# Kernel optimization log

Hardware: AMD Instinct MI355X
Metric: run time of the kernel (lower is better)

## Reference

```python
import jax, jax.numpy as jnp
import numpy as np

B, S, H, DH = 2, 2048, 16, 64
DIM = H * DH          # 1024
WIN = 512             # relpos_win_size
LN_EPS = 1e-5


def setup_inputs() -> dict:
    key = jax.random.key(0)
    ks = jax.random.split(key, 8)
    return {
        "q": jax.random.normal(ks[0], (B, S, H, DH), dtype=jnp.float32),
        "k": jax.random.normal(ks[1], (B, S, H, DH), dtype=jnp.float32),
        "relpos_emb": jax.random.normal(ks[2], (WIN, DIM), dtype=jnp.float32),
        "ln_scale": jnp.ones((DIM,), dtype=jnp.float32),
        "ln_bias": jnp.zeros((DIM,), dtype=jnp.float32),
        "Wq": jax.random.normal(ks[3], (DIM, DIM), dtype=jnp.float32),
        "bq": jnp.zeros((DIM,), dtype=jnp.float32),
        "Wk": jax.random.normal(ks[4], (DIM, DIM), dtype=jnp.float32),
        "bk": jnp.zeros((DIM,), dtype=jnp.float32),
    }


def reference(q, k, relpos_emb, ln_scale, ln_bias, Wq, bq, Wk, bk):
    b, nq, h, dh = q.shape
    nk = k.shape[1]
    win = relpos_emb.shape[0]

    # LayerNorm over the embedding dim (use_pos_layer_norm=True); dropout is identity (eval).
    mu = jnp.mean(relpos_emb, axis=-1, keepdims=True)
    var = jnp.mean(jnp.square(relpos_emb - mu), axis=-1, keepdims=True)
    pe = (relpos_emb - mu) * jax.lax.rsqrt(var + LN_EPS) * ln_scale + ln_bias

    qpos = jnp.arange(nq)
    kpos = jnp.arange(nk)
    rel = jnp.clip(kpos[None, :] - qpos[:, None], -(win - 1), 0) + (win - 1)
    idx = jnp.broadcast_to(rel[None, None, :, :], (b, h, nq, nk))

    # Linear projections of the (small) relpos table, split into heads.
    relpos_k = (pe @ Wk.T + bk).reshape(win, h, dh)  # relpos_k_proj
    relpos_q = (pe @ Wq.T + bq).reshape(win, h, dh)  # relpos_q_proj

    # query-to-position: scores over window then gather along window axis (dim 3).
    query_pos_scores = jnp.einsum('bnhx,khx->bhnk', q, relpos_k)
    logits_query_pos = jnp.take_along_axis(query_pos_scores, idx, axis=3)  # [b,h,nq,nk]

    key_pos_scores = jnp.einsum('bnhx,khx->bhkn', k, relpos_q)
    logits_pos_key = jnp.take_along_axis(key_pos_scores, idx, axis=2)      # [b,h,nq,nk]

    # scale_factor = 1 + True + True = 3 (static constant, omitted from array outputs)
    return logits_pos_key, logits_query_pos, relpos_q, relpos_k
```

## Files before the change

kernel.cpp:

```cpp
#include <hip/hip_runtime.h>

#define BB 2
#define S 2048
#define H 16
#define DH 64
#define DIM 1024
#define WIN 512

#define OUT_PK 0
#define OUT_QP 134217728
#define OUT_RQ 268435456
#define OUT_RK 268959744

#define WS_C0Q   1024
#define WS_C511Q (1024 + 65536)
#define WS_C0K   (1024 + 2*65536)
#define WS_C511K (1024 + 3*65536)
#define WS_BF_BASE 263168

typedef short bf16x8 __attribute__((ext_vector_type(8)));
typedef float f32x4 __attribute__((ext_vector_type(4)));

__device__ inline short f2bf(float f) {
    union { float f; unsigned int u; } cv; cv.f = f;
    unsigned int u = cv.u + 0x7FFFu + ((cv.u >> 16) & 1u);
    return (short)(u >> 16);
}

__device__ inline float bf2f(short s) {
    union { unsigned int u; float f; } cv;
    cv.u = ((unsigned int)(unsigned short)s) << 16;
    return cv.f;
}

__global__ __launch_bounds__(256) void prep1(const float* __restrict__ emb,
        const float* __restrict__ lnsc, const float* __restrict__ lnbi,
        const float* __restrict__ Wq, const float* __restrict__ bq,
        const float* __restrict__ Wk, const float* __restrict__ bk,
        const float* __restrict__ q, const float* __restrict__ k,
        float* __restrict__ out, short* __restrict__ rqbf, short* __restrict__ rkbf,
        short* __restrict__ qbf, short* __restrict__ kbf) {
    __shared__ short As[64 * 72];
    __shared__ short Bs[64 * 72];
    __shared__ float smu[64];
    __shared__ float srs[64];
    int bid = blockIdx.x;
    int t = threadIdx.x;

    if (bid >= 256) {
        int cb = bid - 256;
        int z = cb >> 10;
        int blk = cb & 1023;
        const float* src = z ? k : q;
        short* dst = z ? kbf : qbf;
        int e0 = (blk * 256 + t) * 16;
        int c = e0 & 63, hh = (e0 >> 6) & 15, n = (e0 >> 10) & 2047, b = e0 >> 21;
        short* dbase = dst + (((size_t)(b * 16 + hh) * 2048) + n) * 64 + c;
#pragma unroll
        for (int i = 0; i < 4; ++i) {
            float4 v = *reinterpret_cast<const float4*>(src + e0 + i * 4);
            short4 o = { f2bf(v.x), f2bf(v.y), f2bf(v.z), f2bf(v.w) };
            *reinterpret_cast<short4*>(dbase + i * 4) = o;
        }
        return;
    }

    int z = bid >> 7;
    int d0i = ((bid >> 6) & 1) * 8 + (bid & 7);
    int r0i = (bid >> 3) & 7;
    const float* W    = z ? Wk : Wq;
    const float* bias = z ? bk : bq;
    float* o = out + (z ? OUT_RK : OUT_RQ);
    short* bfo = z ? rkbf : rqbf;
    int r0 = r0i * 64;
    int d0 = d0i * 64;

    {
        int rr = t >> 2, p = t & 3;
        const float4* rp = reinterpret_cast<const float4*>(emb + (r0 + rr) * DIM + p * 256);
        float s = 0.f, sq = 0.f;
#pragma unroll
        for (int i = 0; i < 64; ++i) {
            float4 v = rp[i];
            s  += v.x + v.y + v.z + v.w;
            sq += v.x * v.x + v.y * v.y + v.z * v.z + v.w * v.w;
        }
        s += __shfl_xor(s, 1); sq += __shfl_xor(sq, 1);
        s += __shfl_xor(s, 2); sq += __shfl_xor(sq, 2);
        if (p == 0) {
            float mu = s / DIM;
            float var = sq / DIM - mu * mu;
            smu[rr] = mu;
            srs[rr] = rsqrtf(var + 1e-5f);
        }
    }
    __syncthreads();

    int lane = t & 63, w = t >> 6, lr = lane & 15, lg = lane >> 4;
    int srow = t >> 2, seg = (t & 3) * 16;
    float mu = smu[srow], rs = srs[srow];

    f32x4 acc[4] = {};
    for (int c0 = 0; c0 < DIM; c0 += 64) {
        const float4* ep = reinterpret_cast<const float4*>(emb + (size_t)(r0 + srow) * DIM + c0 + seg);
        const float4* wp = reinterpret_cast<const float4*>(W + (size_t)(d0 + srow) * DIM + c0 + seg);
        short4* ad = reinterpret_cast<short4*>(&As[srow * 72 + seg]);
        short4* wd = reinterpret_cast<short4*>(&Bs[srow * 72 + seg]);
#pragma unroll
        for (int i = 0; i < 4; ++i) {
            float4 v = ep[i], wv = wp[i];
            int cb2 = c0 + seg + i * 4;
            float4 sc = *reinterpret_cast<const float4*>(lnsc + cb2);
            float4 bi = *reinterpret_cast<const float4*>(lnbi + cb2);
            short4 a4 = { f2bf((v.x - mu) * rs * sc.x + bi.x),
                          f2bf((v.y - mu) * rs * sc.y + bi.y),
                          f2bf((v.z - mu) * rs * sc.z + bi.z),
                          f2bf((v.w - mu) * rs * sc.w + bi.w) };
            short4 w4 = { f2bf(wv.x), f2bf(wv.y), f2bf(wv.z), f2bf(wv.w) };
            ad[i] = a4;
            wd[i] = w4;
        }
        __syncthreads();
#pragma unroll
        for (int kk = 0; kk < 2; ++kk) {
            bf16x8 a = *reinterpret_cast<const bf16x8*>(&As[(w * 16 + lr) * 72 + kk * 32 + lg * 8]);
#pragma unroll
            for (int cg = 0; cg < 4; ++cg) {
                bf16x8 b = *reinterpret_cast<const bf16x8*>(&Bs[(cg * 16 + lr) * 72 + kk * 32 + lg * 8]);
                acc[cg] = __builtin_amdgcn_mfma_f32_16x16x32_bf16(a, b, acc[cg], 0, 0, 0);
            }
        }
        __syncthreads();
    }
#pragma unroll
    for (int cg = 0; cg < 4; ++cg) {
        int col = d0 + cg * 16 + lr;
        float bv = bias[col];
        int hh = col >> 6, cc = col & 63;
#pragma unroll
        for (int reg = 0; reg < 4; ++reg) {
            int rr = r0 + w * 16 + lg * 4 + reg;
            float val = acc[cg][reg] + bv;
            o[(size_t)rr * DIM + col] = val;
            bfo[((size_t)(hh * 512) + rr) * 64 + cc] = f2bf(val);
        }
    }
}

__global__ __launch_bounds__(256) void cvec(const short* __restrict__ qbf,
        const short* __restrict__ kbf, const short* __restrict__ rqbf,
        const short* __restrict__ rkbf, float* __restrict__ ws) {
    int cid = blockIdx.x;
    int z = cid >> 10;
    int rem = cid & 1023;
    int bh = rem >> 5, rb = rem & 31;
    int t = threadIdx.x;
    int rr = t >> 2, p = t & 3;
    int n = rb * 64 + rr;
    int h = bh & 15;
    const short* X = (z ? kbf : qbf) + ((size_t)bh * 2048 + n) * 64 + p * 16;
    const short* T = (z ? rqbf : rkbf) + (size_t)h * 512 * 64 + p * 16;
    bf16x8 x0 = *reinterpret_cast<const bf16x8*>(X);
    bf16x8 x1 = *reinterpret_cast<const bf16x8*>(X + 8);
    bf16x8 a0 = *reinterpret_cast<const bf16x8*>(T);
    bf16x8 a1 = *reinterpret_cast<const bf16x8*>(T + 8);
    bf16x8 c0 = *reinterpret_cast<const bf16x8*>(T + 511 * 64);
    bf16x8 c1 = *reinterpret_cast<const bf16x8*>(T + 511 * 64 + 8);
    float d0 = 0.f, d1 = 0.f;
#pragma unroll
    for (int e = 0; e < 8; ++e) {
        float xa = bf2f(x0[e]), xb = bf2f(x1[e]);
        d0 += xa * bf2f(a0[e]) + xb * bf2f(a1[e]);
        d1 += xa * bf2f(c0[e]) + xb * bf2f(c1[e]);
    }
    d0 += __shfl_xor(d0, 1); d0 += __shfl_xor(d0, 2);
    d1 += __shfl_xor(d1, 1); d1 += __shfl_xor(d1, 2);
    if (p == 0) {
        int o = bh * S + n;
        if (!z) { ws[WS_C0Q + o] = d0; ws[WS_C511Q + o] = d1; }
        else    { ws[WS_C0K + o] = d0; ws[WS_C511K + o] = d1; }
    }
}

__global__ __launch_bounds__(256) void outk(const short* __restrict__ qbf,
        const short* __restrict__ kbf, const short* __restrict__ rqbf,
        const short* __restrict__ rkbf, const float* __restrict__ ws,
        float* __restrict__ out) {
    __shared__ short Yt[128 * 68];

    int bid = blockIdx.x;
    int wid = (bid & 7) * 2984 + (bid >> 3);
    int panel = wid / 373, o = wid % 373;
    int PK = panel >> 5, bh = panel & 31, h = bh & 15;
    int t = threadIdx.x;
    float* obase = out + (PK ? OUT_PK : OUT_QP) + (size_t)bh * S * S;

    int nt = 0, rem = o, nL = 0, nB = 0, jlo = 0;
    for (; nt < 32; ++nt) {
        jlo = nt > 8 ? nt - 8 : 0;
        nL = (jlo + 7) >> 3;
        nB = nt - jlo + 1;
        int nR = (38 - nt) >> 3;
        int tot = nL + nB + nR;
        if (rem < tot) break;
        rem -= tot;
    }
    int n0 = nt * 64;

    if (rem < nL || rem >= nL + nB) {
        int left, j0, W;
        if (rem < nL) { left = 1; j0 = rem * 512; W = jlo * 64 - j0; }
        else          { left = 0; int rr = rem - nL - nB; j0 = (nt + 1) * 64 + rr * 512; W = 2048 - j0; }
        if (W > 512) W = 512;
        const float* cv = ws + (PK ? (left ? WS_C0K : WS_C511K)
                                   : (left ? WS_C0Q : WS_C511Q)) + bh * S;
        int w2 = t >> 7;
        int c = (t & 127) * 4;
        int active = c < W;
        if (PK) {
            f32x4 cvv = {0.f, 0.f, 0.f, 0.f};
            if (active) cvv = *reinterpret_cast<const f32x4*>(cv + j0 + c);
#pragma unroll
            for (int i = 0; i < 32; ++i) {
                int n = n0 + w2 * 32 + i;
                if (active)
                    __builtin_nontemporal_store(cvv,
                        reinterpret_cast<f32x4*>(obase + (size_t)n * S + j0 + c));
            }
        } else {
#pragma unroll
            for (int i = 0; i < 32; ++i) {
                int n = n0 + w2 * 32 + i;
                float vs = cv[n];
                f32x4 v = { vs, vs, vs, vs };
                if (active)
                    __builtin_nontemporal_store(v,
                        reinterpret_cast<f32x4*>(obase + (size_t)n * S + j0 + c));
            }
        }
        return;
    }

    int jt = jlo + (rem - nL);
    int j0 = jt * 64;
    int rlo = 511 + j0 - (n0 + 63); rlo = rlo < 0 ? 0 : rlo;

    const short* xb = (PK ? kbf : qbf) + ((size_t)bh * 2048 + (PK ? j0 : n0)) * 64;
    const short* tbase = (PK ? rqbf : rkbf) + (size_t)h * 512 * 64;

    int lane = t & 63, w = t >> 6, lr = lane & 15, lg = lane >> 4;
    const short* arow = xb + (w * 16 + lr) * 64 + lg * 8;
    bf16x8 a0 = *reinterpret_cast<const bf16x8*>(arow);
    bf16x8 a1 = *reinterpret_cast<const bf16x8*>(arow + 32);

    bf16x8 b0s[8], b1s[8];
#pragma unroll
    for (int s = 0; s < 8; ++s) {
        int trow = rlo + s * 16 + lr;
        trow = trow > 511 ? 511 : trow;
        const short* brow = tbase + trow * 64 + lg * 8;
        b0s[s] = *reinterpret_cast<const bf16x8*>(brow);
        b1s[s] = *reinterpret_cast<const bf16x8*>(brow + 32);
    }
#pragma unroll
    for (int s = 0; s < 8; ++s) {
        f32x4 acc = {0.f, 0.f, 0.f, 0.f};
        acc = __builtin_amdgcn_mfma_f32_16x16x32_bf16(a0, b0s[s], acc, 0, 0, 0);
        acc = __builtin_amdgcn_mfma_f32_16x16x32_bf16(a1, b1s[s], acc, 0, 0, 0);
        short4 pk4 = { f2bf(acc[0]), f2bf(acc[1]), f2bf(acc[2]), f2bf(acc[3]) };
        *reinterpret_cast<short4*>(&Yt[(s * 16 + lr) * 68 + w * 16 + lg * 4]) = pk4;
    }
    __syncthreads();

    int tx = t & 15, ty = t >> 4;
#pragma unroll
    for (int i = 0; i < 4; ++i) {
        int rowi = ty + i * 16;
        int n = n0 + rowi;
        float vv[4];
#pragma unroll
        for (int jj = 0; jj < 4; ++jj) {
            int j = j0 + tx * 4 + jj;
            int rel = 511 + j - n;
            rel = rel < 0 ? 0 : (rel > 511 ? 511 : rel);
            int g = rel - rlo;
            int m = PK ? (tx * 4 + jj) : rowi;
            vv[jj] = bf2f(Yt[g * 68 + m]);
        }
        f32x4 v = { vv[0], vv[1], vv[2], vv[3] };
        __builtin_nontemporal_store(v,
            reinterpret_cast<f32x4*>(obase + (size_t)n * S + j0 + tx * 4));
    }
}

extern "C" void kernel_launch(void* const* d_in, const int* in_sizes, int n_in,
                              void* d_out, int out_size, void* d_ws, size_t ws_size,
                              hipStream_t stream) {
    const float* q    = (const float*)d_in[0];
    const float* k    = (const float*)d_in[1];
    const float* emb  = (const float*)d_in[2];
    const float* lnsc = (const float*)d_in[3];
    const float* lnbi = (const float*)d_in[4];
    const float* Wq   = (const float*)d_in[5];
    const float* bq   = (const float*)d_in[6];
    const float* Wk   = (const float*)d_in[7];
    const float* bk   = (const float*)d_in[8];
    float* out = (float*)d_out;
    float* ws  = (float*)d_ws;

    short* qbf  = (short*)(ws + WS_BF_BASE);
    short* kbf  = qbf + (size_t)4194304;
    short* rqbf = kbf + (size_t)4194304;
    short* rkbf = rqbf + (size_t)524288;

    prep1<<<dim3(2304), dim3(256), 0, stream>>>(emb, lnsc, lnbi, Wq, bq, Wk, bk,
                                                q, k, out, rqbf, rkbf, qbf, kbf);
    cvec<<<dim3(2048), dim3(256), 0, stream>>>(qbf, kbf, rqbf, rkbf, ws);
    outk<<<dim3(23872), dim3(256), 0, stream>>>(qbf, kbf, rqbf, rkbf, ws, out);
}
```

Baseline: 226.3 us.

## Split query-pos output into dedicated row-panel kernel computing full score rows

Moves the query-to-position logits onto a separate kernel. Each block computes all 512 window scores for 64 query rows into shared memory, then writes full 2048-wide output rows with constant fills and shifted gathers. This removes the per-tile MFMA recompute and the cvec work for the Q side. The position-to-key path keeps the old tiled kernel. The new kernel uses a large shared-memory buffer (about 66KB) and only 1024 blocks, which lowers occupancy for a store-bound kernel.

```diff
diff --git a/kernel.cpp b/kernel.cpp
--- a/kernel.cpp
+++ b/kernel.cpp
@@ -12,8 +12,6 @@
 #define OUT_RQ 268435456
 #define OUT_RK 268959744
 
-#define WS_C0Q   1024
-#define WS_C511Q (1024 + 65536)
 #define WS_C0K   (1024 + 2*65536)
 #define WS_C511K (1024 + 3*65536)
 #define WS_BF_BASE 263168
@@ -147,19 +145,16 @@
     }
 }
 
-__global__ __launch_bounds__(256) void cvec(const short* __restrict__ qbf,
-        const short* __restrict__ kbf, const short* __restrict__ rqbf,
-        const short* __restrict__ rkbf, float* __restrict__ ws) {
+__global__ __launch_bounds__(256) void cvec_pk(const short* __restrict__ kbf,
+        const short* __restrict__ rqbf, float* __restrict__ ws) {
     int cid = blockIdx.x;
-    int z = cid >> 10;
-    int rem = cid & 1023;
-    int bh = rem >> 5, rb = rem & 31;
+    int bh = cid >> 5, rb = cid & 31;
     int t = threadIdx.x;
     int rr = t >> 2, p = t & 3;
     int n = rb * 64 + rr;
     int h = bh & 15;
-    const short* X = (z ? kbf : qbf) + ((size_t)bh * 2048 + n) * 64 + p * 16;
-    const short* T = (z ? rqbf : rkbf) + (size_t)h * 512 * 64 + p * 16;
+    const short* X = kbf + ((size_t)bh * 2048 + n) * 64 + p * 16;
+    const short* T = rqbf + (size_t)h * 512 * 64 + p * 16;
     bf16x8 x0 = *reinterpret_cast<const bf16x8*>(X);
     bf16x8 x1 = *reinterpret_cast<const bf16x8*>(X + 8);
     bf16x8 a0 = *reinterpret_cast<const bf16x8*>(T);
@@ -177,23 +172,99 @@
     d1 += __shfl_xor(d1, 1); d1 += __shfl_xor(d1, 2);
     if (p == 0) {
         int o = bh * S + n;
-        if (!z) { ws[WS_C0Q + o] = d0; ws[WS_C511Q + o] = d1; }
-        else    { ws[WS_C0K + o] = d0; ws[WS_C511K + o] = d1; }
-    }
-}
-
-__global__ __launch_bounds__(256) void outk(const short* __restrict__ qbf,
-        const short* __restrict__ kbf, const short* __restrict__ rqbf,
-        const short* __restrict__ rkbf, const float* __restrict__ ws,
+        ws[WS_C0K + o] = d0; ws[WS_C511K + o] = d1;
+    }
+}
+
+__global__ __launch_bounds__(256) void qpk(const short* __restrict__ qbf,
+        const short* __restrict__ rkbf, float* __restrict__ out) {
+    __shared__ short Yt[64 * 516];
+
+    int bid = blockIdx.x;
+    int wid = (bid & 7) * 128 + (bid >> 3);
+    int bh = wid >> 5, nt = wid & 31;
+    int h = bh & 15;
+    int n0 = nt * 64;
+    int t = threadIdx.x;
+    int lane = t & 63, w = t >> 6, lr = lane & 15, lg = lane >> 4;
+
+    const short* arow = qbf + ((size_t)bh * 2048 + n0 + w * 16 + lr) * 64 + lg * 8;
+    bf16x8 a0 = *reinterpret_cast<const bf16x8*>(arow);
+    bf16x8 a1 = *reinterpret_cast<const bf16x8*>(arow + 32);
+    const short* tb = rkbf + (size_t)h * 512 * 64 + lr * 64 + lg * 8;
+
+    bf16x8 b0 = *reinterpret_cast<const bf16x8*>(tb);
+    bf16x8 b1 = *reinterpret_cast<const bf16x8*>(tb + 32);
+    for (int s = 0; s < 32; ++s) {
+        bf16x8 nb0 = b0, nb1 = b1;
+        if (s < 31) {
+            const short* nb = tb + (s + 1) * 16 * 64;
+            nb0 = *reinterpret_cast<const bf16x8*>(nb);
+            nb1 = *reinterpret_cast<const bf16x8*>(nb + 32);
+        }
+        f32x4 acc = {0.f, 0.f, 0.f, 0.f};
+        acc = __builtin_amdgcn_mfma_f32_16x16x32_bf16(a0, b0, acc, 0, 0, 0);
+        acc = __builtin_amdgcn_mfma_f32_16x16x32_bf16(a1, b1, acc, 0, 0, 0);
+        int g = s * 16 + lr;
+#pragma unroll
+        for (int reg = 0; reg < 4; ++reg)
+            Yt[(w * 16 + lg * 4 + reg) * 516 + g] = f2bf(acc[reg]);
+        b0 = nb0; b1 = nb1;
+    }
+    __syncthreads();
+
+    float* obase = out + OUT_QP + (size_t)bh * S * S;
+    for (int i = 0; i < 16; ++i) {
+        int m = w * 16 + i;
+        int n = n0 + m;
+        const short* yr = &Yt[m * 516];
+        float v0 = bf2f(yr[0]), v511 = bf2f(yr[511]);
+        int jA = n - 511;
+        int jB = n + 1;
+        int dU = (511 - n) & 3;
+        for (int sg = 0; sg < 8; ++sg) {
+            int j0s = sg * 256;
+            int j = j0s + lane * 4;
+            f32x4 v;
+            if (j0s + 256 <= jA) {
+                v = (f32x4){ v0, v0, v0, v0 };
+            } else if (j0s >= jB) {
+                v = (f32x4){ v511, v511, v511, v511 };
+            } else if (j0s >= jA && j0s + 256 <= jB) {
+                int ab = 511 + j - n - dU;
+                short4 lo = *reinterpret_cast<const short4*>(yr + ab);
+                short4 hi = *reinterpret_cast<const short4*>(yr + ab + 4);
+                short e0, e1, e2, e3;
+                if      (dU == 0) { e0 = lo.x; e1 = lo.y; e2 = lo.z; e3 = lo.w; }
+                else if (dU == 1) { e0 = lo.y; e1 = lo.z; e2 = lo.w; e3 = hi.x; }
+                else if (dU == 2) { e0 = lo.z; e1 = lo.w; e2 = hi.x; e3 = hi.y; }
+                else              { e0 = lo.w; e1 = hi.x; e2 = hi.y; e3 = hi.z; }
+                v = (f32x4){ bf2f(e0), bf2f(e1), bf2f(e2), bf2f(e3) };
+            } else {
+#pragma unroll
+                for (int u = 0; u < 4; ++u) {
+                    int rel = 511 + j + u - n;
+                    rel = rel < 0 ? 0 : (rel > 511 ? 511 : rel);
+                    v[u] = bf2f(yr[rel]);
+                }
+            }
+            __builtin_nontemporal_store(v,
+                reinterpret_cast<f32x4*>(obase + (size_t)n * S + j));
+        }
+    }
+}
+
+__global__ __launch_bounds__(256) void pkk(const short* __restrict__ kbf,
+        const short* __restrict__ rqbf, const float* __restrict__ ws,
         float* __restrict__ out) {
     __shared__ short Yt[128 * 68];
 
     int bid = blockIdx.x;
-    int wid = (bid & 7) * 2984 + (bid >> 3);
-    int panel = wid / 373, o = wid % 373;
-    int PK = panel >> 5, bh = panel & 31, h = bh & 15;
+    int wid = (bid & 7) * 1492 + (bid >> 3);
+    int bh = wid / 373, o = wid % 373;
+    int h = bh & 15;
     int t = threadIdx.x;
-    float* obase = out + (PK ? OUT_PK : OUT_QP) + (size_t)bh * S * S;
+    float* obase = out + OUT_PK + (size_t)bh * S * S;
 
     int nt = 0, rem = o, nL = 0, nB = 0, jlo = 0;
     for (; nt < 32; ++nt) {
@@ -212,31 +283,18 @@
         if (rem < nL) { left = 1; j0 = rem * 512; W = jlo * 64 - j0; }
         else          { left = 0; int rr = rem - nL - nB; j0 = (nt + 1) * 64 + rr * 512; W = 2048 - j0; }
         if (W > 512) W = 512;
-        const float* cv = ws + (PK ? (left ? WS_C0K : WS_C511K)
-                                   : (left ? WS_C0Q : WS_C511Q)) + bh * S;
+        const float* cv = ws + (left ? WS_C0K : WS_C511K) + bh * S;
         int w2 = t >> 7;
         int c = (t & 127) * 4;
         int active = c < W;
-        if (PK) {
-            f32x4 cvv = {0.f, 0.f, 0.f, 0.f};
-            if (active) cvv = *reinterpret_cast<const f32x4*>(cv + j0 + c);
-#pragma unroll
-            for (int i = 0; i < 32; ++i) {
-                int n = n0 + w2 * 32 + i;
-                if (active)
-                    __builtin_nontemporal_store(cvv,
-                        reinterpret_cast<f32x4*>(obase + (size_t)n * S + j0 + c));
-            }
-        } else {
-#pragma unroll
-            for (int i = 0; i < 32; ++i) {
-                int n = n0 + w2 * 32 + i;
-                float vs = cv[n];
-                f32x4 v = { vs, vs, vs, vs };
-                if (active)
-                    __builtin_nontemporal_store(v,
-                        reinterpret_cast<f32x4*>(obase + (size_t)n * S + j0 + c));
-            }
+        f32x4 cvv = {0.f, 0.f, 0.f, 0.f};
+        if (active) cvv = *reinterpret_cast<const f32x4*>(cv + j0 + c);
+#pragma unroll
+        for (int i = 0; i < 32; ++i) {
+            int n = n0 + w2 * 32 + i;
+            if (active)
+                __builtin_nontemporal_store(cvv,
+                    reinterpret_cast<f32x4*>(obase + (size_t)n * S + j0 + c));
         }
         return;
     }
@@ -245,8 +303,8 @@
     int j0 = jt * 64;
     int rlo = 511 + j0 - (n0 + 63); rlo = rlo < 0 ? 0 : rlo;
 
-    const short* xb = (PK ? kbf : qbf) + ((size_t)bh * 2048 + (PK ? j0 : n0)) * 64;
-    const short* tbase = (PK ? rqbf : rkbf) + (size_t)h * 512 * 64;
+    const short* xb = kbf + ((size_t)bh * 2048 + j0) * 64;
+    const short* tbase = rqbf + (size_t)h * 512 * 64;
 
     int lane = t & 63, w = t >> 6, lr = lane & 15, lg = lane >> 4;
     const short* arow = xb + (w * 16 + lr) * 64 + lg * 8;
@@ -284,7 +342,7 @@
             int rel = 511 + j - n;
             rel = rel < 0 ? 0 : (rel > 511 ? 511 : rel);
             int g = rel - rlo;
-            int m = PK ? (tx * 4 + jj) : rowi;
+            int m = tx * 4 + jj;
             vv[jj] = bf2f(Yt[g * 68 + m]);
         }
         f32x4 v = { vv[0], vv[1], vv[2], vv[3] };
@@ -315,6 +373,7 @@
 
     prep1<<<dim3(2304), dim3(256), 0, stream>>>(emb, lnsc, lnbi, Wq, bq, Wk, bk,
                                                 q, k, out, rqbf, rkbf, qbf, kbf);
-    cvec<<<dim3(2048), dim3(256), 0, stream>>>(qbf, kbf, rqbf, rkbf, ws);
-    outk<<<dim3(23872), dim3(256), 0, stream>>>(qbf, kbf, rqbf, rkbf, ws, out);
-}
+    cvec_pk<<<dim3(1024), dim3(256), 0, stream>>>(kbf, rqbf, ws);
+    qpk<<<dim3(1024), dim3(256), 0, stream>>>(qbf, rkbf, out);
+    pkk<<<dim3(11936), dim3(256), 0, stream>>>(kbf, rqbf, ws, out);
+}
```

After: 260.1 us. +14.9%, slower.
